# Kernel optimization log

Hardware: AMD Instinct MI355X
Metric: run time of the kernel (lower is better)

Reference implementation:

```python
import jax, jax.numpy as jnp
import numpy as np

NB_OBJ = 5
DIM_BODY = 10
DIM_OBJ = 15
N_PERM = NB_OBJ * (NB_OBJ - 1)  # 20
LOG_STD_MIN, LOG_STD_MAX = -20.0, 2.0


def _linear_init(key, fan_in, fan_out):
    k1, k2 = jax.random.split(key)
    lim = 1.0 / np.sqrt(fan_in)
    W = jax.random.uniform(k1, (fan_in, fan_out), minval=-lim, maxval=lim, dtype=jnp.float32)
    b = jax.random.uniform(k2, (fan_out,), minval=-lim, maxval=lim, dtype=jnp.float32)
    return W, b


def setup_inputs() -> dict:
    key = jax.random.key(0)
    ks = jax.random.split(key, 12)
    B = 16384
    # graph structure (constants)
    perms = [(i, j) for i in range(NB_OBJ) for j in range(NB_OBJ) if i != j]
    src = jnp.array([p[0] for p in perms], dtype=jnp.int32)   # [E]
    dst = jnp.array([p[1] for p in perms], dtype=jnp.int32)   # [E]
    inc = jnp.array([[k for k, p in enumerate(perms) if p[1] == i] for i in range(NB_OBJ)], dtype=jnp.int32)  # [O,4]
    pred = jnp.arange(2 * N_PERM, dtype=jnp.int32).reshape(N_PERM, 2)  # predicate ids per edge
    # parameters
    mp_W1, mp_b1 = _linear_init(ks[0], 8, 256)
    mp_W2, mp_b2 = _linear_init(ks[1], 256, 128)
    ea_W, ea_b = _linear_init(ks[2], 128, 1)
    phi_W1, phi_b1 = _linear_init(ks[3], 153, 256)
    phi_W2, phi_b2 = _linear_init(ks[4], 256, 128)
    sa_W, sa_b = _linear_init(ks[5], 128, 1)
    rho_W1, rho_b1 = _linear_init(ks[6], 128, 256)
    mean_W, mean_b = _linear_init(ks[7], 256, 4)
    ls_W, ls_b = _linear_init(ks[8], 256, 4)
    obs = jax.random.normal(ks[9], (B, DIM_BODY + NB_OBJ * DIM_OBJ), dtype=jnp.float32)
    ag = jax.random.normal(ks[10], (B, 2 * N_PERM), dtype=jnp.float32)
    g = jax.random.normal(ks[11], (B, 2 * N_PERM), dtype=jnp.float32)
    return dict(obs=obs, ag=ag, g=g,
                mp_W1=mp_W1, mp_b1=mp_b1, mp_W2=mp_W2, mp_b2=mp_b2,
                ea_W=ea_W, ea_b=ea_b,
                phi_W1=phi_W1, phi_b1=phi_b1, phi_W2=phi_W2, phi_b2=phi_b2,
                sa_W=sa_W, sa_b=sa_b,
                rho_W1=rho_W1, rho_b1=rho_b1,
                mean_W=mean_W, mean_b=mean_b, ls_W=ls_W, ls_b=ls_b,
                src=src, dst=dst, inc=inc, pred=pred)


def reference(obs, ag, g,
              mp_W1, mp_b1, mp_W2, mp_b2,
              ea_W, ea_b,
              phi_W1, phi_b1, phi_W2, phi_b2,
              sa_W, sa_b,
              rho_W1, rho_b1,
              mean_W, mean_b, ls_W, ls_b,
              src, dst, inc, pred):
    B = obs.shape[0]
    body = obs[:, :DIM_BODY]                                    # [B,10]
    objs = obs[:, DIM_BODY:].reshape(B, NB_OBJ, DIM_OBJ)        # [B,O,15]
    delta_g = g - ag                                            # [B,40]
    # --- message passing over edges (vectorized gather + cat) ---
    e_pred = delta_g[:, pred]                                   # [B,E,2]
    e_src = objs[:, src, :3]                                    # [B,E,3]
    e_dst = objs[:, dst, :3]                                    # [B,E,3]
    inp_mp = jnp.concatenate([e_pred, e_src, e_dst], axis=-1)   # [B,E,8]
    h = jax.nn.relu(inp_mp @ mp_W1 + mp_b1)
    mp_out = jax.nn.relu(h @ mp_W2 + mp_b2)                     # [B,E,128]
    # --- edge self-attention pooling per object over incoming edges ---
    per_obj = mp_out[:, inc]                                    # [B,O,K,128]
    w = jax.nn.softmax(per_obj @ ea_W + ea_b, axis=2)           # softmax over incoming set
    edge_feat = jnp.sum(w * per_obj, axis=2)                    # [B,O,128]
    # --- deep-set phi over objects ---
    body_rep = jnp.broadcast_to(body[:, None, :], (B, NB_OBJ, DIM_BODY))
    inp = jnp.concatenate([body_rep, objs, edge_feat], axis=-1)  # [B,O,153]
    ph = jax.nn.relu(inp @ phi_W1 + phi_b1)
    phi_out = jax.nn.relu(ph @ phi_W2 + phi_b2)                  # [B,O,128]
    aw = jax.nn.softmax(phi_out @ sa_W + sa_b, axis=1)           # softmax over objects
    pooled = jnp.sum(aw * phi_out, axis=1)                       # [B,128]
    # --- rho actor head ---
    r = jax.nn.relu(pooled @ rho_W1 + rho_b1)
    mean = r @ mean_W + mean_b
    logstd = jnp.clip(r @ ls_W + ls_b, LOG_STD_MIN, LOG_STD_MAX)
    return mean, logstd
```

## Files before the change

### kernel.cpp

```cpp
#include <hip/hip_runtime.h>
#include <cstdint>
#include <cstddef>

typedef unsigned short u16;
typedef unsigned int u32;
typedef __attribute__((ext_vector_type(8))) short bf16x8;
typedef __attribute__((ext_vector_type(4))) float f32x4;

#define MFMA16(A, B, C) __builtin_amdgcn_mfma_f32_16x16x32_bf16((A), (B), (C), 0, 0, 0)

__device__ __forceinline__ u16 bf16_rne(float x) {
    u32 u = __float_as_uint(x);
    u += 0x7fffu + ((u >> 16) & 1u);
    return (u16)(u >> 16);
}
__device__ __forceinline__ float bf2f(u16 h) { return __uint_as_float((u32)h << 16); }
__device__ __forceinline__ u16 bf16_lo(float x, u16 hi) { return bf16_rne(x - bf2f(hi)); }
__device__ __forceinline__ float blo(u32 u) { return __uint_as_float(u << 16); }
__device__ __forceinline__ float bhi(u32 u) { return __uint_as_float(u & 0xffff0000u); }
__device__ __forceinline__ u32 cvt_pk(float a, float b) {
    u32 r;
    asm("v_cvt_pk_bf16_f32 %0, %1, %2" : "=v"(r) : "v"(a), "v"(b));
    return r;
}

__device__ __forceinline__ void PK_body(int tid,
    const float* __restrict__ mpW1, const float* __restrict__ mpW2,
    const float* __restrict__ phW1, const float* __restrict__ phW2,
    const float* __restrict__ rhoW,
    u16* __restrict__ Bp1e, u16* __restrict__ Bp2e,
    u16* __restrict__ BpC1, u16* __restrict__ BpC2, u16* __restrict__ BpR)
{
    if (tid < 8192) {
        int t = tid >> 9, r = tid & 511;
        int l = r >> 3, i = r & 7, g = l >> 4, l15 = l & 15;
        float w = mpW1[i * 256 + 16 * t + l15];
        u16 h = bf16_rne(w);
        Bp1e[tid] = (g < 2) ? h : bf16_lo(w, h);
    } else if (tid < 73728) {
        int f = tid - 8192;
        int b5 = f >> 9, r = f & 511;
        int l = r >> 3, i = r & 7, g = l >> 4, l15 = l & 15;
        int s = b5 & 1, cn = b5 >> 1, c = cn >> 3, n = cn & 7;
        int kk = 32 * c + 8 * g + i;
        float w = mpW2[kk * 128 + 16 * n + l15];
        u16 h = bf16_rne(w);
        Bp2e[f] = s ? bf16_lo(w, h) : h;
    } else if (tid < 155648) {
        int f = tid - 73728;
        int b5 = f >> 9, r = f & 511;
        int l = r >> 3, i = r & 7, g = l >> 4, l15 = l & 15;
        int t = b5 & 15, cs = b5 >> 4, s = cs & 1, c = cs >> 1;
        int kk = 32 * c + 8 * g + i;
        int kp = kk < 25 ? kk : (kk < 32 ? -1 : kk - 7);
        float w = (kp < 0) ? 0.0f : phW1[kp * 256 + 16 * t + l15];
        u16 h = bf16_rne(w);
        BpC1[f] = s ? bf16_lo(w, h) : h;
    } else if (tid < 221184) {
        int f = tid - 155648;
        int b5 = f >> 9, r = f & 511;
        int l = r >> 3, i = r & 7, g = l >> 4, l15 = l & 15;
        int s = b5 & 1, cn = b5 >> 1, c = cn >> 3, n = cn & 7;
        int kk = 32 * c + 8 * g + i;
        float w = phW2[kk * 128 + 16 * n + l15];
        u16 h = bf16_rne(w);
        BpC2[f] = s ? bf16_lo(w, h) : h;
    } else {
        int f = tid - 221184;
        int b5 = f >> 9, r = f & 511;
        int l = r >> 3, i = r & 7, g = l >> 4, l15 = l & 15;
        int s = b5 & 1, ct = b5 >> 1, c = ct >> 4, t = ct & 15;
        int kk = 32 * c + 8 * g + i;
        float w = rhoW[kk * 256 + 16 * t + l15];
        u16 h = bf16_rne(w);
        BpR[f] = s ? bf16_lo(w, h) : h;
    }
}

__device__ __forceinline__ void P1_body(int row,
    const float* __restrict__ obs, const float* __restrict__ ag, const float* __restrict__ g,
    const int* __restrict__ src, const int* __restrict__ dst, const int* __restrict__ pred,
    u16* __restrict__ Ein)
{
    int b = row / 20, p = row - b * 20;
    float inp[8];
    int i0 = pred[2 * p], i1 = pred[2 * p + 1];
    const float* gb = g + (size_t)b * 40;
    const float* ab = ag + (size_t)b * 40;
    inp[0] = gb[i0] - ab[i0];
    inp[1] = gb[i1] - ab[i1];
    int so = src[p], dd = dst[p];
    const float* ob = obs + (size_t)b * 85 + 10;
    inp[2] = ob[so * 15 + 0]; inp[3] = ob[so * 15 + 1]; inp[4] = ob[so * 15 + 2];
    inp[5] = ob[dd * 15 + 0]; inp[6] = ob[dd * 15 + 1]; inp[7] = ob[dd * 15 + 2];

    u32 wh[4], wl[4];
    #pragma unroll
    for (int k = 0; k < 4; ++k) {
        u16 h0 = bf16_rne(inp[2 * k]), h1 = bf16_rne(inp[2 * k + 1]);
        u16 l0 = bf16_lo(inp[2 * k], h0), l1 = bf16_lo(inp[2 * k + 1], h1);
        wh[k] = (u32)h0 | ((u32)h1 << 16);
        wl[k] = (u32)l0 | ((u32)l1 << 16);
    }
    uint4* d4 = (uint4*)(Ein + (size_t)row * 16);
    d4[0] = make_uint4(wh[0], wh[1], wh[2], wh[3]);
    d4[1] = make_uint4(wl[0], wl[1], wl[2], wl[3]);
}

__global__ __launch_bounds__(256) void PREP(
    const float* __restrict__ mpW1, const float* __restrict__ mpW2,
    const float* __restrict__ phW1, const float* __restrict__ phW2,
    const float* __restrict__ rhoW,
    u16* __restrict__ Bp1e, u16* __restrict__ Bp2e,
    u16* __restrict__ BpC1, u16* __restrict__ BpC2, u16* __restrict__ BpR,
    const float* __restrict__ obs, const float* __restrict__ ag, const float* __restrict__ g,
    const int* __restrict__ src, const int* __restrict__ dst, const int* __restrict__ pred,
    u16* __restrict__ Ein,
    const float* __restrict__ meanW, const float* __restrict__ lsW,
    float* __restrict__ headWpk)
{
    int bid = blockIdx.x;
    if (bid < 1120) {
        PK_body(bid * 256 + threadIdx.x, mpW1, mpW2, phW1, phW2, rhoW, Bp1e, Bp2e, BpC1, BpC2, BpR);
    } else if (bid < 2400) {
        P1_body((bid - 1120) * 256 + threadIdx.x, obs, ag, g, src, dst, pred, Ein);
    } else {
        int idx = threadIdx.x;
        #pragma unroll
        for (int r = 0; r < 8; ++r) {
            int f = r * 256 + idx;
            int k = f >> 3, q = f & 7;
            headWpk[f] = (q < 4) ? meanW[k * 4 + q] : lsW[k * 4 + (q - 4)];
        }
    }
}

__global__ __launch_bounds__(512) void GA(
    const u16* __restrict__ Ein, const u16* __restrict__ Bp1, const u16* __restrict__ Bp2,
    const float* __restrict__ b1, const float* __restrict__ b2,
    const float* __restrict__ eaW, const float* __restrict__ eab,
    const int* __restrict__ inc, const float* __restrict__ obs,
    u16* __restrict__ Nin)
{
    __shared__ u16 hb[4][16 * 256];
    __shared__ u16 mpb[80 * 128];
    __shared__ float spart[8][80];
    __shared__ float wbuf[80];
    __shared__ int rowb[80];
    __shared__ int incL[20];

    const int tid = threadIdx.x;
    const int w = tid >> 6, lane = tid & 63;
    const int l15 = lane & 15, gq = lane >> 4;
    const int rowbase = blockIdx.x * 80;
    char* hbc = (char*)hb;
    char* mpc = (char*)mpb;

    if (tid < 20) incL[tid] = inc[tid];

    bf16x8 B1[2];
    float4 b1v[2];
    #pragma unroll
    for (int t = 0; t < 2; ++t) {
        B1[t] = *(const bf16x8*)(Bp1 + (size_t)(2 * w + t) * 512 + lane * 8);
        b1v[t] = *(const float4*)(b1 + 16 * (2 * w + t) + 4 * gq);
    }
    bf16x8 B2[8];
    #pragma unroll
    for (int c = 0; c < 8; ++c)
        B2[c] = *(const bf16x8*)(Bp2 + (size_t)((c * 8 + w) * 2) * 512 + lane * 8);
    const float4 b2v = *(const float4*)(b2 + 16 * w + 4 * gq);
    const float4 eav = *(const float4*)(eaW + 16 * w + 4 * gq);

    auto ldX = [&](int m) {
        return *(const bf16x8*)(Ein + (size_t)(rowbase + m * 16 + l15) * 16 + 8 * (gq & 1));
    };
    auto stage1 = [&](int buf, const bf16x8& X) {
        #pragma unroll
        for (int t = 0; t < 2; ++t) {
            f32x4 acc = {b1v[t].x, b1v[t].y, b1v[t].z, b1v[t].w};
            acc = MFMA16(B1[t], X, acc);
            u32 p0 = cvt_pk(fmaxf(acc[0], 0.f), fmaxf(acc[1], 0.f));
            u32 p1 = cvt_pk(fmaxf(acc[2], 0.f), fmaxf(acc[3], 0.f));
            int colu = 16 * (2 * w + t) + 4 * gq;
            int byte = buf * 8192 + ((l15 * 512 + colu * 2) ^ ((l15 & 7) << 4));
            *(uint2*)(hbc + byte) = make_uint2(p0, p1);
        }
    };
    auto stage2 = [&](int m, int buf) {
        f32x4 accA = {b2v.x, b2v.y, b2v.z, b2v.w};
        f32x4 accB = {0.f, 0.f, 0.f, 0.f};
        #pragma unroll
        for (int c = 0; c < 4; ++c) {
            int byteA = buf * 8192 + ((l15 * 512 + (2 * c) * 64 + gq * 16) ^ ((l15 & 7) << 4));
            int byteB = buf * 8192 + ((l15 * 512 + (2 * c + 1) * 64 + gq * 16) ^ ((l15 & 7) << 4));
            const bf16x8 HA = *(const bf16x8*)(hbc + byteA);
            const bf16x8 HB = *(const bf16x8*)(hbc + byteB);
            accA = MFMA16(B2[2 * c], HA, accA);
            accB = MFMA16(B2[2 * c + 1], HB, accB);
        }
        float v0 = fmaxf(accA[0] + accB[0], 0.f), v1 = fmaxf(accA[1] + accB[1], 0.f);
        float v2 = fmaxf(accA[2] + accB[2], 0.f), v3 = fmaxf(accA[3] + accB[3], 0.f);
        float ep = v0 * eav.x + v1 * eav.y + v2 * eav.z + v3 * eav.w;
        ep += __shfl_xor(ep, 16, 64);
        ep += __shfl_xor(ep, 32, 64);
        if (gq == 0) spart[w][m * 16 + l15] = ep;
        u32 p0 = cvt_pk(v0, v1), p1 = cvt_pk(v2, v3);
        int r = m * 16 + l15;
        int byte2 = (r * 256 + (16 * w + 4 * gq) * 2) ^ ((r & 15) << 4);
        *(uint2*)(mpc + byte2) = make_uint2(p0, p1);
    };

    {
        bf16x8 X0 = ldX(0);
        bf16x8 X1 = ldX(1);
        stage1(0, X0);
        stage1(1, X1);
    }
    __syncthreads();
    {
        bf16x8 X2 = ldX(2);
        bf16x8 X3 = ldX(3);
        stage2(0, 0);
        stage2(1, 1);
        stage1(2, X2);
        stage1(3, X3);
    }
    __syncthreads();
    {
        bf16x8 X4 = ldX(4);
        stage2(2, 2);
        stage2(3, 3);
        stage1(0, X4);
    }
    __syncthreads();
    stage2(4, 0);
    __syncthreads();

    if (tid < 20) {
        int bl = tid / 5, o = tid - bl * 5;
        const float e0 = eab[0];
        int rr[4]; float ee[4];
        #pragma unroll
        for (int i = 0; i < 4; ++i) {
            rr[i] = bl * 20 + incL[o * 4 + i];
            float e = e0;
            #pragma unroll
            for (int ww = 0; ww < 8; ++ww) e += spart[ww][rr[i]];
            ee[i] = e;
        }
        float mx = fmaxf(fmaxf(ee[0], ee[1]), fmaxf(ee[2], ee[3]));
        float ex[4]; float den = 0.f;
        #pragma unroll
        for (int i = 0; i < 4; ++i) { ex[i] = __expf(ee[i] - mx); den += ex[i]; }
        float inv = 1.0f / den;
        #pragma unroll
        for (int i = 0; i < 4; ++i) {
            wbuf[tid * 4 + i] = ex[i] * inv;
            rowb[tid * 4 + i] = rr[i];
        }
    } else if (tid >= 320 && tid < 480) {
        int t2 = tid - 320;
        int p = t2 >> 3, q = t2 & 7;
        int bl = p / 5, o = p - bl * 5;
        const float* body = obs + (size_t)(blockIdx.x * 4 + bl) * 85;
        const float* op = body + 10 + o * 15;
        float v[4];
        #pragma unroll
        for (int jj = 0; jj < 4; ++jj) {
            int col = 4 * q + jj;
            v[jj] = (col < 10) ? body[col] : (col < 25) ? op[col - 10] : 0.0f;
        }
        int grow = blockIdx.x * 20 + p;
        *(uint2*)(Nin + (size_t)grow * 160 + 4 * q) =
            make_uint2(cvt_pk(v[0], v[1]), cvt_pk(v[2], v[3]));
    }
    __syncthreads();

    if (tid < 320) {
        int p = tid >> 4, cb = tid & 15;
        float acc[8] = {0, 0, 0, 0, 0, 0, 0, 0};
        #pragma unroll
        for (int i = 0; i < 4; ++i) {
            int r = rowb[p * 4 + i];
            float wi = wbuf[p * 4 + i];
            int byte = (r * 256 + cb * 16) ^ ((r & 15) << 4);
            uint4 v = *(const uint4*)(mpc + byte);
            acc[0] = fmaf(wi, blo(v.x), acc[0]);
            acc[1] = fmaf(wi, bhi(v.x), acc[1]);
            acc[2] = fmaf(wi, blo(v.y), acc[2]);
            acc[3] = fmaf(wi, bhi(v.y), acc[3]);
            acc[4] = fmaf(wi, blo(v.z), acc[4]);
            acc[5] = fmaf(wi, bhi(v.z), acc[5]);
            acc[6] = fmaf(wi, blo(v.w), acc[6]);
            acc[7] = fmaf(wi, bhi(v.w), acc[7]);
        }
        uint4 ov;
        ov.x = cvt_pk(acc[0], acc[1]);
        ov.y = cvt_pk(acc[2], acc[3]);
        ov.z = cvt_pk(acc[4], acc[5]);
        ov.w = cvt_pk(acc[6], acc[7]);
        int grow = blockIdx.x * 20 + p;
        *(uint4*)(Nin + (size_t)grow * 160 + 32 + cb * 8) = ov;
    }
}

__global__ __launch_bounds__(512) void GB(
    const u16* __restrict__ Nin, const u16* __restrict__ BpC1, const u16* __restrict__ BpC2,
    const u16* __restrict__ BpR,
    const float* __restrict__ b1, const float* __restrict__ b2,
    const float* __restrict__ saW, const float* __restrict__ sab,
    const float* __restrict__ rhob, const float* __restrict__ headWpk,
    const float* __restrict__ meanb, const float* __restrict__ lsb,
    float* __restrict__ outp)
{
    __shared__ u16 hb[2][16 * 256];
    __shared__ u16 phibuf[80 * 132];
    __shared__ float spart[8][80];
    __shared__ float awb[80];

    const int tid = threadIdx.x;
    const int w = tid >> 6, lane = tid & 63;
    const int l15 = lane & 15, gq = lane >> 4;
    const int rowbase = blockIdx.x * 80;
    char* hbc = (char*)hb;
    float* rbuf = (float*)phibuf;
    float* hpart = (float*)spart;
    u32* poolw = (u32*)hb;

    bf16x8 BC[5][2];
    float4 b1v[2];
    #pragma unroll
    for (int t = 0; t < 2; ++t) b1v[t] = *(const float4*)(b1 + 16 * (2 * w + t) + 4 * gq);
    #pragma unroll
    for (int c = 0; c < 5; ++c)
        #pragma unroll
        for (int t = 0; t < 2; ++t)
            BC[c][t] = *(const bf16x8*)(BpC1 + (size_t)((c * 2) * 16 + 2 * w + t) * 512 + lane * 8);
    bf16x8 B2[8];
    #pragma unroll
    for (int c = 0; c < 8; ++c)
        B2[c] = *(const bf16x8*)(BpC2 + (size_t)((c * 8 + w) * 2) * 512 + lane * 8);
    const float4 b2v = *(const float4*)(b2 + 16 * w + 4 * gq);
    const float4 sav = *(const float4*)(saW + 16 * w + 4 * gq);

    auto loadX = [&](int m, bf16x8* X) {
        #pragma unroll
        for (int c = 0; c < 5; ++c)
            X[c] = *(const bf16x8*)(Nin + (size_t)(rowbase + m * 16 + l15) * 160 + 32 * c + 8 * gq);
    };
    auto stage1 = [&](int buf, const bf16x8* X) {
        f32x4 a0 = {b1v[0].x, b1v[0].y, b1v[0].z, b1v[0].w};
        f32x4 a1 = {b1v[1].x, b1v[1].y, b1v[1].z, b1v[1].w};
        #pragma unroll
        for (int c = 0; c < 5; ++c) {
            a0 = MFMA16(BC[c][0], X[c], a0);
            a1 = MFMA16(BC[c][1], X[c], a1);
        }
        #pragma unroll
        for (int t = 0; t < 2; ++t) {
            const f32x4& a = t ? a1 : a0;
            u32 p0 = cvt_pk(fmaxf(a[0], 0.f), fmaxf(a[1], 0.f));
            u32 p1 = cvt_pk(fmaxf(a[2], 0.f), fmaxf(a[3], 0.f));
            int colu = 16 * (2 * w + t) + 4 * gq;
            int byte = buf * 8192 + ((l15 * 512 + colu * 2) ^ ((l15 & 7) << 4));
            *(uint2*)(hbc + byte) = make_uint2(p0, p1);
        }
    };
    auto stage2 = [&](int m, int buf) {
        f32x4 accA = {b2v.x, b2v.y, b2v.z, b2v.w};
        f32x4 accB = {0.f, 0.f, 0.f, 0.f};
        #pragma unroll
        for (int c = 0; c < 4; ++c) {
            int byteA = buf * 8192 + ((l15 * 512 + (2 * c) * 64 + gq * 16) ^ ((l15 & 7) << 4));
            int byteB = buf * 8192 + ((l15 * 512 + (2 * c + 1) * 64 + gq * 16) ^ ((l15 & 7) << 4));
            const bf16x8 HA = *(const bf16x8*)(hbc + byteA);
            const bf16x8 HB = *(const bf16x8*)(hbc + byteB);
            accA = MFMA16(B2[2 * c], HA, accA);
            accB = MFMA16(B2[2 * c + 1], HB, accB);
        }
        float v0 = fmaxf(accA[0] + accB[0], 0.f), v1 = fmaxf(accA[1] + accB[1], 0.f);
        float v2 = fmaxf(accA[2] + accB[2], 0.f), v3 = fmaxf(accA[3] + accB[3], 0.f);
        int r = m * 16 + l15;
        *(uint2*)((char*)phibuf + r * 264 + (16 * w + 4 * gq) * 2) =
            make_uint2(cvt_pk(v0, v1), cvt_pk(v2, v3));
        float sp = v0 * sav.x + v1 * sav.y + v2 * sav.z + v3 * sav.w;
        sp += __shfl_xor(sp, 16, 64);
        sp += __shfl_xor(sp, 32, 64);
        if (gq == 0) spart[w][r] = sp;
    };

    bf16x8 Xc[5];
    loadX(0, Xc);
    stage1(0, Xc);
    __syncthreads();
    #pragma unroll 1
    for (int m = 0; m < 5; ++m) {
        bf16x8 Xn[5];
        if (m < 4) loadX(m + 1, Xn);
        stage2(m, m & 1);
        if (m < 4) stage1((m + 1) & 1, Xn);
        __syncthreads();
    }

    if (tid < 16) {
        const float s0c = sab[0];
        float ss[5];
        #pragma unroll
        for (int o = 0; o < 5; ++o) {
            float s = s0c;
            #pragma unroll
            for (int ww = 0; ww < 8; ++ww) s += spart[ww][tid * 5 + o];
            ss[o] = s;
        }
        float mx = fmaxf(fmaxf(fmaxf(ss[0], ss[1]), fmaxf(ss[2], ss[3])), ss[4]);
        float ex[5]; float den = 0.f;
        #pragma unroll
        for (int o = 0; o < 5; ++o) { ex[o] = __expf(ss[o] - mx); den += ex[o]; }
        float inv = 1.0f / den;
        #pragma unroll
        for (int o = 0; o < 5; ++o) awb[tid * 5 + o] = ex[o] * inv;
    }
    __syncthreads();

    #pragma unroll
    for (int rep = 0; rep < 2; ++rep) {
        int idx = rep * 512 + tid;
        int b = idx >> 6, cw = idx & 63;
        float p0 = 0.f, p1 = 0.f;
        #pragma unroll
        for (int o = 0; o < 5; ++o) {
            u32 v = *(const u32*)((const char*)phibuf + (size_t)(b * 5 + o) * 264 + cw * 4);
            float a = awb[b * 5 + o];
            p0 = fmaf(a, blo(v), p0);
            p1 = fmaf(a, bhi(v), p1);
        }
        u16 h0 = bf16_rne(p0); u16 l0 = bf16_lo(p0, h0);
        u16 h1 = bf16_rne(p1); u16 l1 = bf16_lo(p1, h1);
        *(uint2*)(poolw + b * 132 + 2 * cw) =
            make_uint2((u32)h0 | ((u32)l0 << 16), (u32)h1 | ((u32)l1 << 16));
    }
    __syncthreads();

    {
        float4 rb0 = *(const float4*)(rhob + 16 * (2 * w + 0) + 4 * gq);
        float4 rb1 = *(const float4*)(rhob + 16 * (2 * w + 1) + 4 * gq);
        f32x4 acc0 = {rb0.x, rb0.y, rb0.z, rb0.w};
        f32x4 acc1 = {rb1.x, rb1.y, rb1.z, rb1.w};
        #pragma unroll
        for (int c = 0; c < 4; ++c) {
            uint4 q0 = *(const uint4*)(poolw + l15 * 132 + 32 * c + 8 * gq);
            uint4 q1 = *(const uint4*)(poolw + l15 * 132 + 32 * c + 8 * gq + 4);
            u32 ws[8] = {q0.x, q0.y, q0.z, q0.w, q1.x, q1.y, q1.z, q1.w};
            bf16x8 Ph, Pl;
            #pragma unroll
            for (int i = 0; i < 8; ++i) {
                Ph[i] = (short)(ws[i] & 0xffffu);
                Pl[i] = (short)(ws[i] >> 16);
            }
            #pragma unroll
            for (int t = 0; t < 2; ++t) {
                bf16x8 Bh = *(const bf16x8*)(BpR + (size_t)((c * 16 + 2 * w + t) * 2 + 0) * 512 + lane * 8);
                f32x4& a = t ? acc1 : acc0;
                a = MFMA16(Bh, Ph, a);
                a = MFMA16(Bh, Pl, a);
            }
        }
        #pragma unroll
        for (int t = 0; t < 2; ++t) {
            const f32x4& a = t ? acc1 : acc0;
            float4 v;
            v.x = fmaxf(a[0], 0.f); v.y = fmaxf(a[1], 0.f);
            v.z = fmaxf(a[2], 0.f); v.w = fmaxf(a[3], 0.f);
            *(float4*)(rbuf + l15 * 260 + 16 * (2 * w + t) + 4 * gq) = v;
        }
    }
    __syncthreads();

    {
        int s = tid >> 7, p = tid & 127;
        int b = p >> 3, q = p & 7;
        const float* rrow = rbuf + b * 260 + s * 64;
        const float* wcol = headWpk + s * 64 * 8 + q;
        float acc = 0.f;
        #pragma unroll 8
        for (int k = 0; k < 64; ++k)
            acc = fmaf(rrow[k], wcol[k * 8], acc);
        hpart[s * 128 + p] = acc;
    }
    __syncthreads();
    if (tid < 128) {
        int b = tid >> 3, q = tid & 7;
        float a = hpart[tid] + hpart[128 + tid] + hpart[256 + tid] + hpart[384 + tid];
        int bg = blockIdx.x * 16 + b;
        if (q < 4) {
            outp[(size_t)bg * 4 + q] = a + meanb[q];
        } else {
            float l = a + lsb[q - 4];
            outp[65536 + (size_t)bg * 4 + (q - 4)] = fminf(fmaxf(l, -20.0f), 2.0f);
        }
    }
}

extern "C" void kernel_launch(void* const* d_in, const int* in_sizes, int n_in,
                              void* d_out, int out_size, void* d_ws, size_t ws_size,
                              hipStream_t stream)
{
    const float* obs   = (const float*)d_in[0];
    const float* ag    = (const float*)d_in[1];
    const float* g     = (const float*)d_in[2];
    const float* mpW1  = (const float*)d_in[3];
    const float* mpb1  = (const float*)d_in[4];
    const float* mpW2  = (const float*)d_in[5];
    const float* mpb2  = (const float*)d_in[6];
    const float* eaW   = (const float*)d_in[7];
    const float* eab   = (const float*)d_in[8];
    const float* phW1  = (const float*)d_in[9];
    const float* phb1  = (const float*)d_in[10];
    const float* phW2  = (const float*)d_in[11];
    const float* phb2  = (const float*)d_in[12];
    const float* saW   = (const float*)d_in[13];
    const float* sab   = (const float*)d_in[14];
    const float* rhoW  = (const float*)d_in[15];
    const float* rhob  = (const float*)d_in[16];
    const float* meanW = (const float*)d_in[17];
    const float* meanb = (const float*)d_in[18];
    const float* lsW   = (const float*)d_in[19];
    const float* lsb   = (const float*)d_in[20];
    const int*   src   = (const int*)d_in[21];
    const int*   dst   = (const int*)d_in[22];
    const int*   inc   = (const int*)d_in[23];
    const int*   pred  = (const int*)d_in[24];

    char* ws = (char*)d_ws;
    u16* Ein  = (u16*)(ws + 0);
    u16* Nin  = (u16*)(ws + 10485760ull);
    u16* Bp1e = (u16*)(ws + 36700160ull);
    u16* Bp2e = (u16*)(ws + 36716544ull);
    u16* BpC1 = (u16*)(ws + 36847616ull);
    u16* BpC2 = (u16*)(ws + 37011456ull);
    u16* BpR  = (u16*)(ws + 37142528ull);
    float* headWpk = (float*)(ws + 37273600ull);

    hipLaunchKernelGGL(PREP, dim3(2401), dim3(256), 0, stream,
                       mpW1, mpW2, phW1, phW2, rhoW, Bp1e, Bp2e, BpC1, BpC2, BpR,
                       obs, ag, g, src, dst, pred, Ein, meanW, lsW, headWpk);
    hipLaunchKernelGGL(GA, dim3(4096), dim3(512), 0, stream,
                       Ein, Bp1e, Bp2e, mpb1, mpb2, eaW, eab, inc, obs, Nin);
    hipLaunchKernelGGL(GB, dim3(1024), dim3(512), 0, stream,
                       Nin, BpC1, BpC2, BpR, phb1, phb2, saW, sab, rhob,
                       headWpk, meanb, lsb, (float*)d_out);
}
```

Before: 106.9 us.

## Process two row-tiles per barrier phase in GB with quad-buffered hidden LDS

Doubles the shared hidden-activation buffer from two to four slots and unrolls the 5-tile loop so two tiles run stage1/stage2 between each barrier. This cuts the number of __syncthreads from six to four and gives more independent MFMA work per phase. In exchange it uses more LDS, which may lower occupancy, and raises register pressure from holding two X tiles at once.

```diff
diff --git a/kernel.cpp b/kernel.cpp
--- a/kernel.cpp
+++ b/kernel.cpp
@@ -314,7 +314,7 @@
     const float* __restrict__ meanb, const float* __restrict__ lsb,
     float* __restrict__ outp)
 {
-    __shared__ u16 hb[2][16 * 256];
+    __shared__ u16 hb[4][16 * 256];
     __shared__ u16 phibuf[80 * 132];
     __shared__ float spart[8][80];
     __shared__ float awb[80];
@@ -390,18 +390,34 @@
         if (gq == 0) spart[w][r] = sp;
     };
 
-    bf16x8 Xc[5];
-    loadX(0, Xc);
-    stage1(0, Xc);
-    __syncthreads();
-    #pragma unroll 1
-    for (int m = 0; m < 5; ++m) {
-        bf16x8 Xn[5];
-        if (m < 4) loadX(m + 1, Xn);
-        stage2(m, m & 1);
-        if (m < 4) stage1((m + 1) & 1, Xn);
-        __syncthreads();
-    }
+    {
+        bf16x8 X0[5], X1[5];
+        loadX(0, X0);
+        loadX(1, X1);
+        stage1(0, X0);
+        stage1(1, X1);
+    }
+    __syncthreads();
+    {
+        bf16x8 X2[5], X3[5];
+        loadX(2, X2);
+        loadX(3, X3);
+        stage2(0, 0);
+        stage2(1, 1);
+        stage1(2, X2);
+        stage1(3, X3);
+    }
+    __syncthreads();
+    {
+        bf16x8 X4[5];
+        loadX(4, X4);
+        stage2(2, 2);
+        stage2(3, 3);
+        stage1(0, X4);
+    }
+    __syncthreads();
+    stage2(4, 0);
+    __syncthreads();
 
     if (tid < 16) {
         const float s0c = sab[0];
```

New measurement: 97.43 us, median of 2. 8.9% less time.
